# Performance work log

Hardware: AMD Instinct MI355X
Metric: run time of the kernel (lower is better)

The kernel has to match this reference:

```python
import jax, jax.numpy as jnp
import numpy as np

WINDOW_SIZE = 11
CHANNEL = 3
SIGMA = 1.5
C1 = 0.01 ** 2
C2 = 0.03 ** 2


def _create_window(window_size: int, channel: int) -> jnp.ndarray:
    coords = jnp.arange(window_size, dtype=jnp.float32) - window_size // 2
    g = jnp.exp(-coords ** 2 / (2 * SIGMA ** 2))
    g = g / g.sum()
    w2d = jnp.outer(g, g)  # [K, K]
    # depthwise conv kernel, OIHW with O=channel, I=1
    return jnp.broadcast_to(w2d, (channel, 1, window_size, window_size))


def _depthwise_conv(x, window):
    pad = WINDOW_SIZE // 2
    return jax.lax.conv_general_dilated(
        x, window,
        window_strides=(1, 1),
        padding=[(pad, pad), (pad, pad)],
        dimension_numbers=("NCHW", "OIHW", "NCHW"),
        feature_group_count=x.shape[1],
    )


def setup_inputs() -> dict:
    key = jax.random.key(0)
    k1, k2 = jax.random.split(key)
    pred = jax.random.uniform(k1, (16, 3, 512, 512), dtype=jnp.float32)
    target = jax.random.uniform(k2, (16, 3, 512, 512), dtype=jnp.float32)
    window = _create_window(WINDOW_SIZE, CHANNEL)
    return {"pred": pred, "target": target, "window": window}


def reference(pred, target, window):
    mu1 = _depthwise_conv(pred, window)
    mu2 = _depthwise_conv(target, window)
    mu1_sq = mu1 * mu1
    mu2_sq = mu2 * mu2
    mu1_mu2 = mu1 * mu2
    sigma1_sq = _depthwise_conv(pred * pred, window) - mu1_sq
    sigma2_sq = _depthwise_conv(target * target, window) - mu2_sq
    sigma12 = _depthwise_conv(pred * target, window) - mu1_mu2
    ssim_map = ((2 * mu1_mu2 + C1) * (2 * sigma12 + C2)) / (
        (mu1_sq + mu2_sq + C1) * (sigma1_sq + sigma2_sq + C2)
    )
    return 1.0 - ssim_map.mean()
```

## Files before the change

### kernel.cpp

```cpp
#include <hip/hip_runtime.h>
#include <hip/hip_bf16.h>

#define IMG_H 512
#define IMG_W 512
#define IMG_N (IMG_H * IMG_W)
#define NPLANES 48
#define TILE 64
#define XS 88
#define SSIM_C1 0.0001f
#define SSIM_C2 0.0009f

typedef __attribute__((ext_vector_type(8))) short bf16x8;
typedef __attribute__((ext_vector_type(4))) float f32x4;

__device__ __forceinline__ unsigned bf16r(float x) {
    unsigned u = __float_as_uint(x);
    return (u + 0x7fffu + ((u >> 16) & 1u)) >> 16;
}
__device__ __forceinline__ unsigned pk2(float a, float b) {
    return bf16r(a) | (bf16r(b) << 16);
}
__device__ __forceinline__ float lo16(unsigned u) { return __uint_as_float(u << 16); }
__device__ __forceinline__ float hi16(unsigned u) { return __uint_as_float(u & 0xffff0000u); }
__device__ __forceinline__ unsigned sqpk(unsigned u) {
    float a = lo16(u), b = hi16(u); return pk2(a * a, b * b);
}
__device__ __forceinline__ unsigned mulpk(unsigned u, unsigned v) {
    return pk2(lo16(u) * lo16(v), hi16(u) * hi16(v));
}

__global__ __launch_bounds__(256) void ssim_mfma_kernel(
    const float* __restrict__ pred, const float* __restrict__ target,
    const float* __restrict__ window, float* __restrict__ partial)
{
    __shared__ unsigned short Xp[80 * XS];
    __shared__ unsigned short Xt[80 * XS];
    __shared__ unsigned short Ht[64 * XS];
    __shared__ unsigned short gbfS[16];
    __shared__ float wsum[4];

    const int tid  = threadIdx.x;
    const int w    = tid >> 6;
    const int lane = tid & 63;
    const int n15  = lane & 15;
    const int quad = lane >> 4;

    if (tid < 16) {
        float gv = 0.f;
        if (tid < 11) {
            float s = 0.f;
            #pragma unroll
            for (int j = 0; j < 11; ++j) s += window[tid * 11 + j];
            gv = s;
        }
        gbfS[tid] = (unsigned short)bf16r(gv);
    }

    const int plane  = blockIdx.z;
    const int base_r = blockIdx.y * TILE;
    const int base_c = blockIdx.x * TILE;
    const float* pp = pred   + (size_t)plane * IMG_N;
    const float* tp = target + (size_t)plane * IMG_N;

    #pragma unroll
    for (int i = 0; i < 7; ++i) {
        const unsigned fi = (unsigned)tid + 256u * i;
        if (fi < 1600u) {
            const unsigned ri = fi / 20u, q = fi - 20u * ri;
            const int gr = base_r - 8 + (int)ri;
            const int gc = base_c - 8 + 4 * (int)q;
            const bool ok = ((unsigned)gr < (unsigned)IMG_H) &&
                            ((unsigned)gc < (unsigned)IMG_W);
            const float4 z4 = make_float4(0.f, 0.f, 0.f, 0.f);
            float4 p4 = ok ? *(const float4*)(pp + gr * IMG_W + gc) : z4;
            float4 t4 = ok ? *(const float4*)(tp + gr * IMG_W + gc) : z4;
            const int off = (int)ri * XS + 4 * (int)q;
            *(uint2*)&Xp[off] = make_uint2(pk2(p4.x, p4.y), pk2(p4.z, p4.w));
            *(uint2*)&Xt[off] = make_uint2(pk2(t4.x, t4.y), pk2(t4.z, t4.w));
        }
    }
    __syncthreads();

    uint4 wu;
    {
        unsigned wd[4];
        #pragma unroll
        for (int d = 0; d < 4; ++d) {
            const int t0 = 8 * quad + 2 * d - n15 - 3;
            const unsigned lo = gbfS[((unsigned)t0       <= 10u) ? t0       : 11];
            const unsigned hi = gbfS[((unsigned)(t0 + 1) <= 10u) ? (t0 + 1) : 11];
            wd[d] = lo | (hi << 16);
        }
        wu = make_uint4(wd[0], wd[1], wd[2], wd[3]);
    }
    const bf16x8 wfrag = __builtin_bit_cast(bf16x8, wu);
    const f32x4 zero4 = {0.f, 0.f, 0.f, 0.f};

    f32x4 vacc[5][4];
    #pragma unroll
    for (int c = 0; c < 5; ++c)
        #pragma unroll
        for (int r = 0; r < 4; ++r) vacc[c][r] = zero4;

    #pragma unroll
    for (int ch = 0; ch < 5; ++ch) {
        #pragma unroll
        for (int rt = 0; rt < 5; ++rt) {
            const int xoff = (16 * rt + n15) * XS + 16 * w + 8 * quad;
            uint4 pu, tu, au;
            if (ch != 1 && ch != 3) pu = *(const uint4*)&Xp[xoff];
            if (ch != 0 && ch != 2) tu = *(const uint4*)&Xt[xoff];
            if      (ch == 0) au = pu;
            else if (ch == 1) au = tu;
            else if (ch == 2) au = make_uint4(sqpk(pu.x), sqpk(pu.y), sqpk(pu.z), sqpk(pu.w));
            else if (ch == 3) au = make_uint4(sqpk(tu.x), sqpk(tu.y), sqpk(tu.z), sqpk(tu.w));
            else              au = make_uint4(mulpk(pu.x, tu.x), mulpk(pu.y, tu.y),
                                              mulpk(pu.z, tu.z), mulpk(pu.w, tu.w));
            const bf16x8 afrag = __builtin_bit_cast(bf16x8, au);
            const f32x4 hd = __builtin_amdgcn_mfma_f32_16x16x32_bf16(
                afrag, wfrag, zero4, 0, 0, 0);
            *(uint2*)&Ht[(16 * w + n15) * XS + 16 * rt + 4 * quad] =
                make_uint2(pk2(hd[0], hd[1]), pk2(hd[2], hd[3]));
        }
        #pragma unroll
        for (int rt = 0; rt < 4; ++rt) {
            const bf16x8 bfrag = *(const bf16x8*)&Ht[(16 * w + n15) * XS +
                                                     16 * rt + 8 * quad];
            vacc[ch][rt] = __builtin_amdgcn_mfma_f32_16x16x32_bf16(
                wfrag, bfrag, vacc[ch][rt], 0, 0, 0);
        }
    }

    float acc = 0.f;
    #pragma unroll
    for (int rt = 0; rt < 4; ++rt) {
        #pragma unroll
        for (int r = 0; r < 4; ++r) {
            const float mu1 = vacc[0][rt][r], mu2 = vacc[1][rt][r];
            const float e11 = vacc[2][rt][r], e22 = vacc[3][rt][r];
            const float e12 = vacc[4][rt][r];
            const float mu1_sq = mu1 * mu1, mu2_sq = mu2 * mu2;
            const float mu1_mu2 = mu1 * mu2;
            const float s1  = e11 - mu1_sq;
            const float s2  = e22 - mu2_sq;
            const float s12 = e12 - mu1_mu2;
            const float num = (2.f * mu1_mu2 + SSIM_C1) * (2.f * s12 + SSIM_C2);
            const float den = (mu1_sq + mu2_sq + SSIM_C1) * (s1 + s2 + SSIM_C2);
            acc += num * __builtin_amdgcn_rcpf(den);
        }
    }

    #pragma unroll
    for (int off = 32; off > 0; off >>= 1)
        acc += __shfl_down(acc, off, 64);
    if (lane == 0) wsum[w] = acc;
    __syncthreads();
    if (tid == 0) {
        const int bid = blockIdx.x + gridDim.x * (blockIdx.y + gridDim.y * blockIdx.z);
        partial[bid] = wsum[0] + wsum[1] + wsum[2] + wsum[3];
    }
}

__global__ __launch_bounds__(256) void ssim_reduce_kernel(
    const float* __restrict__ partial, float* __restrict__ out)
{
    const int tid = threadIdx.x;
    float s = 0.f;
    #pragma unroll
    for (int k = 0; k < 12; ++k) s += partial[tid + 256 * k];
    double acc = (double)s;
    #pragma unroll
    for (int off = 32; off > 0; off >>= 1)
        acc += __shfl_down(acc, off, 64);
    __shared__ double wsumd[4];
    const int lane = tid & 63, wid = tid >> 6;
    if (lane == 0) wsumd[wid] = acc;
    __syncthreads();
    if (tid == 0) {
        const double total = wsumd[0] + wsumd[1] + wsumd[2] + wsumd[3];
        const double N = (double)NPLANES * IMG_H * IMG_W;
        out[0] = (float)(1.0 - total / N);
    }
}

extern "C" void kernel_launch(void* const* d_in, const int* in_sizes, int n_in,
                              void* d_out, int out_size, void* d_ws, size_t ws_size,
                              hipStream_t stream)
{
    const float* pred   = (const float*)d_in[0];
    const float* target = (const float*)d_in[1];
    const float* window = (const float*)d_in[2];
    float* out = (float*)d_out;
    float* partial = (float*)d_ws;

    dim3 grid(IMG_W / TILE, IMG_H / TILE, NPLANES);
    ssim_mfma_kernel<<<grid, 256, 0, stream>>>(pred, target, window, partial);
    ssim_reduce_kernel<<<1, 256, 0, stream>>>(partial, out);
}
```

Measured before the change: 156.0 us.

## Replace LDS staging of horizontal pass with ds_bpermute register shuffles

Removes the shared-memory Ht buffer that held the horizontal-conv intermediate. The horizontal MFMA outputs stay in registers and are rearranged into B fragments with ds_bpermute cross-lane shuffles. The vertical pass now runs two MFMAs per output tile, using half-zeroed weight fragments over the previous and current horizontal tiles, in a rolling loop that fuses all five channels with the SSIM epilogue. This cuts LDS footprint and LDS write/read traffic and should raise occupancy, at the cost of more permute instructions and extra MFMAs.

New measurement: 153.3 us. No clear change (-1.7%).

```diff
diff --git a/kernel.cpp b/kernel.cpp
--- a/kernel.cpp
+++ b/kernel.cpp
@@ -35,7 +35,6 @@
 {
     __shared__ unsigned short Xp[80 * XS];
     __shared__ unsigned short Xt[80 * XS];
-    __shared__ unsigned short Ht[64 * XS];
     __shared__ unsigned short gbfS[16];
     __shared__ float wsum[4];
 
@@ -93,52 +92,67 @@
         }
         wu = make_uint4(wd[0], wd[1], wd[2], wd[3]);
     }
-    const bf16x8 wfrag = __builtin_bit_cast(bf16x8, wu);
+    const uint4 zu = make_uint4(0u, 0u, 0u, 0u);
+    const bf16x8 wfrag  = __builtin_bit_cast(bf16x8, wu);
+    const bf16x8 wfragL = __builtin_bit_cast(bf16x8, (quad < 2) ? wu : zu);
+    const bf16x8 wfragH = __builtin_bit_cast(bf16x8, (quad < 2) ? zu : wu);
     const f32x4 zero4 = {0.f, 0.f, 0.f, 0.f};
 
-    f32x4 vacc[5][4];
-    #pragma unroll
-    for (int c = 0; c < 5; ++c)
-        #pragma unroll
-        for (int r = 0; r < 4; ++r) vacc[c][r] = zero4;
-
-    #pragma unroll
-    for (int ch = 0; ch < 5; ++ch) {
-        #pragma unroll
-        for (int rt = 0; rt < 5; ++rt) {
-            const int xoff = (16 * rt + n15) * XS + 16 * w + 8 * quad;
-            uint4 pu, tu, au;
-            if (ch != 1 && ch != 3) pu = *(const uint4*)&Xp[xoff];
-            if (ch != 0 && ch != 2) tu = *(const uint4*)&Xt[xoff];
+    const int idxA = 4 * (32 * (quad & 1) + n15);
+    const int idxB = idxA + 64;
+
+    auto h_tile = [&](int h, unsigned (&P)[5][2]) {
+        const int xoff = (16 * h + n15) * XS + 16 * w + 8 * quad;
+        const uint4 pu = *(const uint4*)&Xp[xoff];
+        const uint4 tu = *(const uint4*)&Xt[xoff];
+        #pragma unroll
+        for (int ch = 0; ch < 5; ++ch) {
+            uint4 au;
             if      (ch == 0) au = pu;
             else if (ch == 1) au = tu;
-            else if (ch == 2) au = make_uint4(sqpk(pu.x), sqpk(pu.y), sqpk(pu.z), sqpk(pu.w));
-            else if (ch == 3) au = make_uint4(sqpk(tu.x), sqpk(tu.y), sqpk(tu.z), sqpk(tu.w));
+            else if (ch == 2) au = make_uint4(sqpk(pu.x), sqpk(pu.y),
+                                              sqpk(pu.z), sqpk(pu.w));
+            else if (ch == 3) au = make_uint4(sqpk(tu.x), sqpk(tu.y),
+                                              sqpk(tu.z), sqpk(tu.w));
             else              au = make_uint4(mulpk(pu.x, tu.x), mulpk(pu.y, tu.y),
                                               mulpk(pu.z, tu.z), mulpk(pu.w, tu.w));
-            const bf16x8 afrag = __builtin_bit_cast(bf16x8, au);
             const f32x4 hd = __builtin_amdgcn_mfma_f32_16x16x32_bf16(
-                afrag, wfrag, zero4, 0, 0, 0);
-            *(uint2*)&Ht[(16 * w + n15) * XS + 16 * rt + 4 * quad] =
-                make_uint2(pk2(hd[0], hd[1]), pk2(hd[2], hd[3]));
-        }
-        #pragma unroll
-        for (int rt = 0; rt < 4; ++rt) {
-            const bf16x8 bfrag = *(const bf16x8*)&Ht[(16 * w + n15) * XS +
-                                                     16 * rt + 8 * quad];
-            vacc[ch][rt] = __builtin_amdgcn_mfma_f32_16x16x32_bf16(
-                wfrag, bfrag, vacc[ch][rt], 0, 0, 0);
-        }
-    }
+                __builtin_bit_cast(bf16x8, au), wfrag, zero4, 0, 0, 0);
+            P[ch][0] = pk2(hd[0], hd[1]);
+            P[ch][1] = pk2(hd[2], hd[3]);
+        }
+    };
+
+    auto bfrag_of = [&](const unsigned* Pch) -> bf16x8 {
+        uint4 b;
+        b.x = (unsigned)__builtin_amdgcn_ds_bpermute(idxA, (int)Pch[0]);
+        b.y = (unsigned)__builtin_amdgcn_ds_bpermute(idxA, (int)Pch[1]);
+        b.z = (unsigned)__builtin_amdgcn_ds_bpermute(idxB, (int)Pch[0]);
+        b.w = (unsigned)__builtin_amdgcn_ds_bpermute(idxB, (int)Pch[1]);
+        return __builtin_bit_cast(bf16x8, b);
+    };
+
+    unsigned Pprev[5][2], Pcur[5][2];
+    h_tile(0, Pprev);
 
     float acc = 0.f;
     #pragma unroll
     for (int rt = 0; rt < 4; ++rt) {
+        h_tile(rt + 1, Pcur);
+        f32x4 s[5];
+        #pragma unroll
+        for (int ch = 0; ch < 5; ++ch) {
+            const bf16x8 bP = bfrag_of(Pprev[ch]);
+            const bf16x8 bC = bfrag_of(Pcur[ch]);
+            f32x4 t = __builtin_amdgcn_mfma_f32_16x16x32_bf16(
+                wfragL, bP, zero4, 0, 0, 0);
+            s[ch] = __builtin_amdgcn_mfma_f32_16x16x32_bf16(
+                wfragH, bC, t, 0, 0, 0);
+        }
         #pragma unroll
         for (int r = 0; r < 4; ++r) {
-            const float mu1 = vacc[0][rt][r], mu2 = vacc[1][rt][r];
-            const float e11 = vacc[2][rt][r], e22 = vacc[3][rt][r];
-            const float e12 = vacc[4][rt][r];
+            const float mu1 = s[0][r], mu2 = s[1][r];
+            const float e11 = s[2][r], e22 = s[3][r], e12 = s[4][r];
             const float mu1_sq = mu1 * mu1, mu2_sq = mu2 * mu2;
             const float mu1_mu2 = mu1 * mu2;
             const float s1  = e11 - mu1_sq;
@@ -147,6 +161,11 @@
             const float num = (2.f * mu1_mu2 + SSIM_C1) * (2.f * s12 + SSIM_C2);
             const float den = (mu1_sq + mu2_sq + SSIM_C1) * (s1 + s2 + SSIM_C2);
             acc += num * __builtin_amdgcn_rcpf(den);
+        }
+        #pragma unroll
+        for (int ch = 0; ch < 5; ++ch) {
+            Pprev[ch][0] = Pcur[ch][0];
+            Pprev[ch][1] = Pcur[ch][1];
         }
     }
 
```

## Keep horizontal-pass results in registers and switch SSIM MFMA path to fp16

Applied to the files above, without the earlier changes.

The horizontal Gaussian pass output now feeds the vertical pass straight from registers. Two 16x16x16 f16 MFMAs with shifted weight fragments consume the previous and current row tiles, which removes the LDS Ht write/read round trip. The staging, square and product computations switch from bf16 with manual rounding to fp16 using cvt_pkrtz and packed half multiplies, which cuts ALU work. In exchange, fp16 gives a smaller exponent range and round-toward-zero conversion, and the rolling Pprev/Pcur buffers add register pressure.

Result: faster. 144.6 us (-7.3%).

```diff
diff --git a/kernel.cpp b/kernel.cpp
--- a/kernel.cpp
+++ b/kernel.cpp
@@ -1,5 +1,4 @@
 #include <hip/hip_runtime.h>
-#include <hip/hip_bf16.h>
 
 #define IMG_H 512
 #define IMG_W 512
@@ -10,23 +9,17 @@
 #define SSIM_C1 0.0001f
 #define SSIM_C2 0.0009f
 
-typedef __attribute__((ext_vector_type(8))) short bf16x8;
-typedef __attribute__((ext_vector_type(4))) float f32x4;
-
-__device__ __forceinline__ unsigned bf16r(float x) {
-    unsigned u = __float_as_uint(x);
-    return (u + 0x7fffu + ((u >> 16) & 1u)) >> 16;
-}
+typedef _Float16 f16x2 __attribute__((ext_vector_type(2)));
+typedef _Float16 f16x4 __attribute__((ext_vector_type(4)));
+typedef _Float16 f16x8 __attribute__((ext_vector_type(8)));
+typedef float    f32x4 __attribute__((ext_vector_type(4)));
+
 __device__ __forceinline__ unsigned pk2(float a, float b) {
-    return bf16r(a) | (bf16r(b) << 16);
-}
-__device__ __forceinline__ float lo16(unsigned u) { return __uint_as_float(u << 16); }
-__device__ __forceinline__ float hi16(unsigned u) { return __uint_as_float(u & 0xffff0000u); }
-__device__ __forceinline__ unsigned sqpk(unsigned u) {
-    float a = lo16(u), b = hi16(u); return pk2(a * a, b * b);
-}
-__device__ __forceinline__ unsigned mulpk(unsigned u, unsigned v) {
-    return pk2(lo16(u) * lo16(v), hi16(u) * hi16(v));
+    return __builtin_bit_cast(unsigned,
+        __builtin_amdgcn_cvt_pkrtz(a, b));
+}
+__device__ __forceinline__ f16x2 pk2h(float a, float b) {
+    return __builtin_bit_cast(f16x2, __builtin_amdgcn_cvt_pkrtz(a, b));
 }
 
 __global__ __launch_bounds__(256) void ssim_mfma_kernel(
@@ -35,8 +28,7 @@
 {
     __shared__ unsigned short Xp[80 * XS];
     __shared__ unsigned short Xt[80 * XS];
-    __shared__ unsigned short Ht[64 * XS];
-    __shared__ unsigned short gbfS[16];
+    __shared__ unsigned short gfS[16];
     __shared__ float wsum[4];
 
     const int tid  = threadIdx.x;
@@ -53,7 +45,8 @@
             for (int j = 0; j < 11; ++j) s += window[tid * 11 + j];
             gv = s;
         }
-        gbfS[tid] = (unsigned short)bf16r(gv);
+        const _Float16 hg = (_Float16)gv;
+        gfS[tid] = __builtin_bit_cast(unsigned short, hg);
     }
 
     const int plane  = blockIdx.z;
@@ -87,58 +80,71 @@
         #pragma unroll
         for (int d = 0; d < 4; ++d) {
             const int t0 = 8 * quad + 2 * d - n15 - 3;
-            const unsigned lo = gbfS[((unsigned)t0       <= 10u) ? t0       : 11];
-            const unsigned hi = gbfS[((unsigned)(t0 + 1) <= 10u) ? (t0 + 1) : 11];
+            const unsigned lo = gfS[((unsigned)t0       <= 10u) ? t0       : 11];
+            const unsigned hi = gfS[((unsigned)(t0 + 1) <= 10u) ? (t0 + 1) : 11];
             wd[d] = lo | (hi << 16);
         }
         wu = make_uint4(wd[0], wd[1], wd[2], wd[3]);
     }
-    const bf16x8 wfrag = __builtin_bit_cast(bf16x8, wu);
+    const f16x8 wfrag = __builtin_bit_cast(f16x8, wu);
+
+    f16x4 w0frag, w1frag;
+    {
+        unsigned a[2], b[2];
+        #pragma unroll
+        for (int d = 0; d < 2; ++d) {
+            const int k0 = 4 * quad + 2 * d;
+            const int a0 = k0 - n15 - 3,  a1 = a0 + 1;
+            const int b0 = k0 - n15 + 13, b1 = b0 + 1;
+            a[d] = gfS[((unsigned)a0 <= 10u) ? a0 : 11] |
+                   ((unsigned)gfS[((unsigned)a1 <= 10u) ? a1 : 11] << 16);
+            b[d] = gfS[((unsigned)b0 <= 10u) ? b0 : 11] |
+                   ((unsigned)gfS[((unsigned)b1 <= 10u) ? b1 : 11] << 16);
+        }
+        w0frag = __builtin_bit_cast(f16x4, make_uint2(a[0], a[1]));
+        w1frag = __builtin_bit_cast(f16x4, make_uint2(b[0], b[1]));
+    }
     const f32x4 zero4 = {0.f, 0.f, 0.f, 0.f};
 
-    f32x4 vacc[5][4];
-    #pragma unroll
-    for (int c = 0; c < 5; ++c)
-        #pragma unroll
-        for (int r = 0; r < 4; ++r) vacc[c][r] = zero4;
-
-    #pragma unroll
-    for (int ch = 0; ch < 5; ++ch) {
-        #pragma unroll
-        for (int rt = 0; rt < 5; ++rt) {
-            const int xoff = (16 * rt + n15) * XS + 16 * w + 8 * quad;
-            uint4 pu, tu, au;
-            if (ch != 1 && ch != 3) pu = *(const uint4*)&Xp[xoff];
-            if (ch != 0 && ch != 2) tu = *(const uint4*)&Xt[xoff];
+    auto h_tile = [&](int h, f16x4 (&P)[5]) {
+        const int xoff = (16 * h + n15) * XS + 16 * w + 8 * quad;
+        const f16x8 pu = *(const f16x8*)&Xp[xoff];
+        const f16x8 tu = *(const f16x8*)&Xt[xoff];
+        #pragma unroll
+        for (int ch = 0; ch < 5; ++ch) {
+            f16x8 au;
             if      (ch == 0) au = pu;
             else if (ch == 1) au = tu;
-            else if (ch == 2) au = make_uint4(sqpk(pu.x), sqpk(pu.y), sqpk(pu.z), sqpk(pu.w));
-            else if (ch == 3) au = make_uint4(sqpk(tu.x), sqpk(tu.y), sqpk(tu.z), sqpk(tu.w));
-            else              au = make_uint4(mulpk(pu.x, tu.x), mulpk(pu.y, tu.y),
-                                              mulpk(pu.z, tu.z), mulpk(pu.w, tu.w));
-            const bf16x8 afrag = __builtin_bit_cast(bf16x8, au);
-            const f32x4 hd = __builtin_amdgcn_mfma_f32_16x16x32_bf16(
-                afrag, wfrag, zero4, 0, 0, 0);
-            *(uint2*)&Ht[(16 * w + n15) * XS + 16 * rt + 4 * quad] =
-                make_uint2(pk2(hd[0], hd[1]), pk2(hd[2], hd[3]));
-        }
-        #pragma unroll
-        for (int rt = 0; rt < 4; ++rt) {
-            const bf16x8 bfrag = *(const bf16x8*)&Ht[(16 * w + n15) * XS +
-                                                     16 * rt + 8 * quad];
-            vacc[ch][rt] = __builtin_amdgcn_mfma_f32_16x16x32_bf16(
-                wfrag, bfrag, vacc[ch][rt], 0, 0, 0);
-        }
-    }
+            else if (ch == 2) au = pu * pu;
+            else if (ch == 3) au = tu * tu;
+            else              au = pu * tu;
+            const f32x4 hd = __builtin_amdgcn_mfma_f32_16x16x32_f16(
+                au, wfrag, zero4, 0, 0, 0);
+            const f16x2 l  = pk2h(hd[0], hd[1]);
+            const f16x2 hh = pk2h(hd[2], hd[3]);
+            P[ch] = f16x4{l.x, l.y, hh.x, hh.y};
+        }
+    };
+
+    f16x4 Pprev[5], Pcur[5];
+    h_tile(0, Pprev);
 
     float acc = 0.f;
     #pragma unroll
     for (int rt = 0; rt < 4; ++rt) {
+        h_tile(rt + 1, Pcur);
+        f32x4 s[5];
+        #pragma unroll
+        for (int ch = 0; ch < 5; ++ch) {
+            const f32x4 t = __builtin_amdgcn_mfma_f32_16x16x16f16(
+                w0frag, Pprev[ch], zero4, 0, 0, 0);
+            s[ch] = __builtin_amdgcn_mfma_f32_16x16x16f16(
+                w1frag, Pcur[ch], t, 0, 0, 0);
+        }
         #pragma unroll
         for (int r = 0; r < 4; ++r) {
-            const float mu1 = vacc[0][rt][r], mu2 = vacc[1][rt][r];
-            const float e11 = vacc[2][rt][r], e22 = vacc[3][rt][r];
-            const float e12 = vacc[4][rt][r];
+            const float mu1 = s[0][r], mu2 = s[1][r];
+            const float e11 = s[2][r], e22 = s[3][r], e12 = s[4][r];
             const float mu1_sq = mu1 * mu1, mu2_sq = mu2 * mu2;
             const float mu1_mu2 = mu1 * mu2;
             const float s1  = e11 - mu1_sq;
@@ -148,6 +154,8 @@
             const float den = (mu1_sq + mu2_sq + SSIM_C1) * (s1 + s2 + SSIM_C2);
             acc += num * __builtin_amdgcn_rcpf(den);
         }
+        #pragma unroll
+        for (int ch = 0; ch < 5; ++ch) Pprev[ch] = Pcur[ch];
     }
 
     #pragma unroll
```
